# Kernel tuning notes

Measured on AMD Instinct MI355X. Metric: run time of the kernel, lower is better.

Reference implementation:

```python
import jax, jax.numpy as jnp
import numpy as np

MAP_X = 72; MAP_Y = 72      # global map grid
R = 300                      # number of rooms
MAXS = 8                     # rooms padded to 8x8 (zero-padded occupancy)
E = 32                       # room_embedding_width
N = 128                      # batch
CONV_CH = [64, 128, 256]; KS = [5, 3, 3]
FC = [512, 256]; OUT_W = 512


def setup_inputs() -> dict:
    key = jax.random.key(0)
    ks = jax.random.split(key, 20)
    rng = np.random.default_rng(0)
    widths = rng.integers(1, MAXS + 1, R)
    heights = rng.integers(1, MAXS + 1, R)
    # room_maps[i] is room.map transposed -> [width, height], zero-padded to [MAXS, MAXS]
    rm = np.zeros((R, MAXS, MAXS), np.int32)
    for i in range(R):
        rm[i, :widths[i], :heights[i]] = rng.integers(0, 2, (int(widths[i]), int(heights[i])))
    inp = {}
    # room top-left positions; rooms fit since max size is MAXS
    inp["X"] = jax.random.randint(ks[0], (N, R, 2), 0, MAP_X - MAXS + 1, dtype=jnp.int32)
    inp["room_maps"] = jnp.asarray(rm)
    inp["room_emb"] = jax.random.normal(ks[1], (R, E), jnp.float32)
    cin = [1 + E] + CONV_CH
    for i in range(3):
        k = KS[i]; fan = cin[i] * k * k
        inp[f"conv_w{i}"] = jax.random.normal(ks[2 + 2 * i], (cin[i + 1], cin[i], k, k), jnp.float32) / np.sqrt(fan).astype(np.float32)
        inp[f"conv_b{i}"] = jnp.zeros((cin[i + 1],), jnp.float32)
    fcd = [CONV_CH[-1]] + FC + [OUT_W]
    for i in range(3):
        inp[f"fc_w{i}"] = jax.random.normal(ks[10 + 2 * i], (fcd[i + 1], fcd[i]), jnp.float32) / np.sqrt(fcd[i]).astype(np.float32)
        inp[f"fc_b{i}"] = jnp.zeros((fcd[i + 1],), jnp.float32)
    return inp


def _encode_map(X, room_maps, room_emb):
    # Fused scatter: occupancy channel + embedding channels scattered in one pass.
    rm = room_maps.astype(room_emb.dtype)                    # [R, W, H]
    vals = jnp.concatenate(
        [rm[..., None], rm[..., None] * room_emb[:, None, None, :]], axis=-1
    )                                                        # [R, W, H, 1+E]
    ax = jnp.arange(MAXS)

    def one(pos):  # pos: [R, 2] positions for one batch element
        ix = jnp.broadcast_to(pos[:, 0, None, None] + ax[None, :, None], (R, MAXS, MAXS))
        iy = jnp.broadcast_to(pos[:, 1, None, None] + ax[None, None, :], (R, MAXS, MAXS))
        grid = jnp.zeros((MAP_X, MAP_Y, 1 + E), vals.dtype)
        # padded cells are zero so dropped/duplicate adds are exact
        return grid.at[ix, iy].add(vals, mode="drop")

    out = jax.vmap(one)(X)                                   # [N, MAP_X, MAP_Y, 1+E]
    # torch: transpose(1,3) -> [N, 1+E, MAP_Y, MAP_X]
    return jnp.transpose(out, (0, 3, 2, 1))


def _conv_relu(x, w, b, k):
    p = k // 2
    y = jax.lax.conv_general_dilated(
        x, w, (1, 1), [(p, p), (p, p)], dimension_numbers=("NCHW", "OIHW", "NCHW"))
    return jax.nn.relu(y + b[None, :, None, None])


def _maxpool3s2(x):
    return jax.lax.reduce_window(x, -jnp.inf, jax.lax.max, (1, 1, 3, 3), (1, 1, 2, 2), "VALID")


def reference(X, room_maps, room_emb, conv_w0, conv_b0, conv_w1, conv_b1, conv_w2, conv_b2, fc_w0, fc_b0, fc_w1, fc_b1, fc_w2, fc_b2):
    x = _encode_map(X, room_maps, room_emb)
    for w, b, k in ((conv_w0, conv_b0, KS[0]), (conv_w1, conv_b1, KS[1]), (conv_w2, conv_b2, KS[2])):
        x = _maxpool3s2(_conv_relu(x, w, b, k))
    x = jnp.mean(x, axis=(2, 3))                             # GlobalAvgPool2d
    x = jax.nn.relu(x @ fc_w0.T + fc_b0)
    x = jax.nn.relu(x @ fc_w1.T + fc_b1)
    return x @ fc_w2.T + fc_b2
```

## Files before the change

kernel.cpp:

```cpp
#include <hip/hip_runtime.h>
#include <hip/hip_bf16.h>
#include <cstdint>
#include <cstddef>

#define NB      128
#define RR      300
#define EMB     32

typedef __bf16 bf16x8 __attribute__((ext_vector_type(8)));
typedef float  f32x4  __attribute__((ext_vector_type(4)));
typedef unsigned short ushort8 __attribute__((ext_vector_type(8)));

__device__ __forceinline__ unsigned short f2bf(float f) {
    union { __hip_bfloat16 h; unsigned short u; } c;
    c.h = __float2bfloat16(f);
    return c.u;
}
__device__ __forceinline__ float bf2f(unsigned short u) {
    union { __hip_bfloat16 h; unsigned short u; } c;
    c.u = u;
    return __bfloat162float(c.h);
}

__device__ __forceinline__ void wpack_body(
    const float* __restrict__ w, unsigned short* __restrict__ wPT,
    int COUT, int CIN, int KK, int gpc, int idx, int total)
{
    if (idx >= total) return;
    int kk = idx & 31;
    int t  = idx >> 5;
    int oc = t % COUT;
    int kb = t / COUT;
    int g  = kb * 4 + (kk >> 3);
    int j  = kk & 7;
    int shift = g / gpc;
    int ci    = (g % gpc) * 8 + j;
    float v = (shift < KK && ci < CIN)
        ? w[(size_t)oc * CIN * KK + (size_t)ci * KK + shift] : 0.0f;
    wPT[idx] = f2bf(v);
}

__device__ __forceinline__ void fcT_body(
    const float* __restrict__ w, float* __restrict__ wT, int O, int I, int idx)
{
    if (idx >= O * I) return;
    int i = idx % I, o = idx / I;
    wT[(size_t)i * O + o] = w[idx];
}

__global__ __launch_bounds__(256) void prep_k(
    const int* __restrict__ rm, unsigned long long* __restrict__ masks,
    const float* __restrict__ cw0, unsigned short* __restrict__ WP0,
    const float* __restrict__ cw1, unsigned short* __restrict__ WP1,
    const float* __restrict__ cw2, unsigned short* __restrict__ WP2,
    int* __restrict__ kt0, int* __restrict__ kt1, int* __restrict__ kt2,
    const float* __restrict__ fw0, float* __restrict__ W0T,
    const float* __restrict__ fw1, float* __restrict__ W1T,
    const float* __restrict__ fw2, float* __restrict__ W2T)
{
    const int b = blockIdx.x;
    const int t = threadIdx.x;
    if (b < 2) {
        int r = b * 256 + t;
        if (r < RR) {
            unsigned long long m = 0ull;
            #pragma unroll
            for (int k = 0; k < 64; ++k)
                if (rm[r * 64 + k]) m |= (1ull << k);
            masks[r] = m;
        }
    } else if (b < 258) {
        wpack_body(cw0, WP0, 64, 33, 25, 5, (b - 2) * 256 + t, 32 * 64 * 32);
    } else if (b < 546) {
        wpack_body(cw1, WP1, 128, 64, 9, 8, (b - 258) * 256 + t, 18 * 128 * 32);
    } else if (b < 1698) {
        wpack_body(cw2, WP2, 256, 128, 9, 16, (b - 546) * 256 + t, 36 * 256 * 32);
    } else if (b < 1699) {
        #pragma unroll
        for (int which = 0; which < 3; ++which) {
            int ngr, gpc, K, Wp, CL;
            int* dst;
            if (which == 0)      { ngr = 128; gpc = 5;  K = 5; Wp = 20; CL = 40;  dst = kt0; }
            else if (which == 1) { ngr = 72;  gpc = 8;  K = 3; Wp = 37; CL = 72;  dst = kt1; }
            else                 { ngr = 144; gpc = 16; K = 3; Wp = 19; CL = 136; dst = kt2; }
            if (t < ngr) {
                int shift = t / gpc;
                int off = 0;
                if (shift < K * K) {
                    int ky = shift / K, kx = shift % K;
                    off = (ky * Wp + kx) * CL + (t % gpc) * 8;
                }
                dst[t] = off;
            }
        }
    } else if (b < 2211) {
        fcT_body(fw0, W0T, 512, 256, (b - 1699) * 256 + t);
    } else if (b < 2723) {
        fcT_body(fw1, W1T, 256, 512, (b - 2211) * 256 + t);
    } else {
        fcT_body(fw2, W2T, 512, 256, (b - 2723) * 256 + t);
    }
}

__device__ __forceinline__ void border_body(
    unsigned short* __restrict__ base, int Hp, int Wp, int CPG, int pad,
    int sampleStride, int nborder, int idx, int total)
{
    if (idx >= total) return;
    int c8 = idx % CPG;
    int t  = idx / CPG;
    int bi = t % nborder;
    int nl = t / nborder;

    int topN = pad * Wp;
    int y, x;
    if (bi < topN) {
        y = bi / Wp; x = bi - y * Wp;
    } else if (bi < 2 * topN) {
        int b2 = bi - topN;
        y = Hp - pad + b2 / Wp; x = b2 % Wp;
    } else {
        int mid = bi - 2 * topN;
        int rowlen = 2 * pad;
        y = pad + mid / rowlen;
        int r = mid % rowlen;
        x = r < pad ? r : Wp - pad + (r - pad);
    }
    uint4 z = make_uint4(0, 0, 0, 0);
    *reinterpret_cast<uint4*>(
        &base[((size_t)nl * sampleStride) +
              ((size_t)y * Wp + x) * (CPG * 8) + c8 * 8]) = z;
}

__global__ __launch_bounds__(512) void encode_k(
    const int* __restrict__ X, const unsigned long long* __restrict__ masks,
    const float* __restrict__ emb, unsigned short* __restrict__ G,
    int n0, int sampleStride)
{
    __shared__ float tile[4][72][33];
    __shared__ unsigned s_pos[RR];
    __shared__ unsigned long long s_mask[RR];
    __shared__ unsigned short s_list[320];
    __shared__ float s_emb[64 * 33];
    __shared__ int s_woff[8];
    __shared__ int s_cnt;

    const int nl = blockIdx.x, band = blockIdx.y;
    const int by = band * 4;
    const int n  = n0 + nl;
    const int tid = threadIdx.x;

    float* tf = &tile[0][0][0];
    for (int i = tid; i < 4 * 72 * 33; i += 512) tf[i] = 0.0f;

    const int2* Xp = reinterpret_cast<const int2*>(X);
    bool hot = false;
    if (tid < RR) {
        int2 pos = Xp[n * RR + tid];
        s_pos[tid]  = (unsigned)pos.x | ((unsigned)pos.y << 16);
        s_mask[tid] = masks[tid];
        hot = (pos.y <= by + 3) && (pos.y + 7 >= by);
    }
    unsigned long long bal = __ballot(hot);
    if ((tid & 63) == 0) s_woff[tid >> 6] = (int)__popcll(bal);
    __syncthreads();
    if (tid == 0) {
        int acc = 0;
        #pragma unroll
        for (int w = 0; w < 8; ++w) { int c = s_woff[w]; s_woff[w] = acc; acc += c; }
        s_cnt = acc;
    }
    __syncthreads();
    if (hot) {
        int w = tid >> 6, b = tid & 63;
        unsigned long long before = (b == 0) ? 0ull : (bal & ((1ull << b) - 1ull));
        s_list[s_woff[w] + (int)__popcll(before)] = (unsigned short)tid;
    }
    __syncthreads();

    const int lane = tid & 63;
    const int wvi  = tid >> 6;
    const int dx   = lane >> 3;
    const int c0   = (lane & 7) * 5;
    const int cnt  = s_cnt;

    for (int base = 0; base < cnt; base += 64) {
        int cn = cnt - base; if (cn > 64) cn = 64;
        for (int i = tid; i < cn * 33; i += 512) {
            int hi = i / 33, cc = i - hi * 33;
            int r = s_list[base + hi];
            s_emb[i] = (cc == 0) ? 1.0f : emb[r * EMB + cc - 1];
        }
        __syncthreads();

        int j = wvi;
        for (; j + 8 < cn; j += 16) {
            int rA = s_list[base + j];
            int rB = s_list[base + j + 8];
            unsigned pA = s_pos[rA], pB = s_pos[rB];
            unsigned long long mA = s_mask[rA] >> (dx * 8);
            unsigned long long mB = s_mask[rB] >> (dx * 8);
            int xA = (pA & 0xffff) + dx, yA = pA >> 16;
            int xB = (pB & 0xffff) + dx, yB = pB >> 16;
            float eA[5], eB[5];
            #pragma unroll
            for (int q = 0; q < 5; ++q) {
                eA[q] = (c0 + q < 33) ? s_emb[j * 33 + c0 + q] : 0.0f;
                eB[q] = (c0 + q < 33) ? s_emb[(j + 8) * 33 + c0 + q] : 0.0f;
            }
            #pragma unroll
            for (int dyb = 0; dyb < 4; ++dyb) {
                int dA = by + dyb - yA;
                if ((unsigned)dA < 8u && ((mA >> dA) & 1ull)) {
                    #pragma unroll
                    for (int q = 0; q < 5; ++q)
                        if (c0 + q < 33)
                            atomicAdd(&tile[dyb][xA][c0 + q], eA[q]);
                }
                int dB = by + dyb - yB;
                if ((unsigned)dB < 8u && ((mB >> dB) & 1ull)) {
                    #pragma unroll
                    for (int q = 0; q < 5; ++q)
                        if (c0 + q < 33)
                            atomicAdd(&tile[dyb][xB][c0 + q], eB[q]);
                }
            }
        }
        for (; j < cn; j += 8) {
            int r = s_list[base + j];
            unsigned pxy = s_pos[r];
            int px = pxy & 0xffff, py = pxy >> 16;
            unsigned long long mm = s_mask[r] >> (dx * 8);
            int x = px + dx;
            float ev[5];
            #pragma unroll
            for (int q = 0; q < 5; ++q)
                ev[q] = (c0 + q < 33) ? s_emb[j * 33 + c0 + q] : 0.0f;
            #pragma unroll
            for (int dyb = 0; dyb < 4; ++dyb) {
                int dyr = by + dyb - py;
                if ((unsigned)dyr < 8u && ((mm >> dyr) & 1ull)) {
                    #pragma unroll
                    for (int q = 0; q < 5; ++q)
                        if (c0 + q < 33)
                            atomicAdd(&tile[dyb][x][c0 + q], ev[q]);
                }
            }
        }
        __syncthreads();
    }
    __syncthreads();

    unsigned short* Gn = G + (size_t)nl * sampleStride;
    for (int i = tid; i < 4 * 72 * 10; i += 512) {
        int cc = i % 10;
        int t  = i / 10;
        int x  = t % 72;
        int dyb = t / 72;
        int c0w = cc * 4;
        unsigned short r[4];
        #pragma unroll
        for (int j = 0; j < 4; ++j)
            r[j] = (c0w + j < 33) ? f2bf(tile[dyb][x][c0w + j]) : 0;
        uint2 pk;
        pk.x = (unsigned)r[0] | ((unsigned)r[1] << 16);
        pk.y = (unsigned)r[2] | ((unsigned)r[3] << 16);
        *reinterpret_cast<uint2*>(
            &Gn[((size_t)(by + dyb + 2) * 76 + (x + 2)) * 40 + c0w]) = pk;
    }

    uint2 zz; zz.x = 0; zz.y = 0;
    for (int i = tid; i < 160; i += 512) {
        int cc = i % 10;
        int t  = i / 10;
        int ci = t & 3;
        int dyb = t >> 2;
        int x = ci < 2 ? ci : 72 + ci;
        *reinterpret_cast<uint2*>(
            &Gn[((size_t)(by + dyb + 2) * 76 + x) * 40 + cc * 4]) = zz;
    }
    if (band == 0 || band == 17) {
        int rbase = band == 0 ? 0 : 74;
        for (int i = tid; i < 2 * 76 * 10; i += 512) {
            int cc = i % 10;
            int t  = i / 10;
            int x  = t % 76;
            int r  = t / 76;
            *reinterpret_cast<uint2*>(
                &Gn[((size_t)(rbase + r) * 76 + x) * 40 + cc * 4]) = zz;
        }
    }
}

template<int KSTEPS>
__global__ __launch_bounds__(256, 3) void conv0_tile_k(
    const unsigned short* __restrict__ inP,
    const unsigned short* __restrict__ wPT,
    const int* __restrict__ ktab,
    const float* __restrict__ bias,
    unsigned short* __restrict__ out,
    int inSS, int outSS)
{
    constexpr int CL = 40;
    constexpr int LP = 72;
    __shared__ __align__(16) unsigned short slab[28 * 20 * CL];
    __shared__ __align__(16) unsigned short wbuf[2][2048];
    __shared__ int s_kt[KSTEPS * 4];
    unsigned short* s_c = slab;

    const int tid = threadIdx.x;
    const int tl  = blockIdx.x;
    const int nl  = blockIdx.y;
    const int tyi = tl / 5, txi = tl % 5;
    const int y0 = tyi * 24;
    const int x0 = txi < 4 ? txi * 16 : 56;

    const int lane = tid & 63, wv = tid >> 6, frow = lane & 15, fq = lane >> 4;

    if (tid < KSTEPS * 4) s_kt[tid] = ktab[tid];

    {
        const unsigned short* src = wPT + wv * 512 + lane * 8;
        __builtin_amdgcn_global_load_lds(
            (const __attribute__((address_space(1))) void*)src,
            (__attribute__((address_space(3))) void*)&wbuf[0][wv * 512],
            16, 0, 0);
    }

    const unsigned short* in_n = inP + (size_t)nl * inSS;
    {
        const uint4* src = reinterpret_cast<const uint4*>(in_n);
        uint4* dst = reinterpret_cast<uint4*>(slab);
        #pragma unroll
        for (int it = 0; it < 11; ++it) {
            int q = tid + it * 256;
            if (q < 2800) {
                int r = q / 100, c = q - r * 100;
                dst[q] = src[((y0 + r) * 76 + x0) * 5 + c];
            }
        }
    }

    int ldsb[6];
    #pragma unroll
    for (int mf = 0; mf < 6; ++mf)
        ldsb[mf] = ((mf * 4 + wv) * 20 + frow) * CL;

    f32x4 acc[6][4];
    #pragma unroll
    for (int a = 0; a < 6; ++a)
        #pragma unroll
        for (int b = 0; b < 4; ++b) acc[a][b] = (f32x4){0.f, 0.f, 0.f, 0.f};

    __syncthreads();

    #pragma unroll 2
    for (int kb = 0; kb < KSTEPS; ++kb) {
        const int cur = kb & 1;
        if (kb + 1 < KSTEPS) {
            const unsigned short* src =
                wPT + (size_t)(kb + 1) * 2048 + wv * 512 + lane * 8;
            __builtin_amdgcn_global_load_lds(
                (const __attribute__((address_space(1))) void*)src,
                (__attribute__((address_space(3))) void*)&wbuf[cur ^ 1][wv * 512],
                16, 0, 0);
        }
        int go = s_kt[kb * 4 + fq];
        bf16x8 af[6];
        #pragma unroll
        for (int mf = 0; mf < 6; ++mf)
            af[mf] = *reinterpret_cast<const bf16x8*>(&slab[ldsb[mf] + go]);
        const unsigned short* wl = &wbuf[cur][frow * 32 + fq * 8];
        #pragma unroll
        for (int ng = 0; ng < 4; ++ng) {
            bf16x8 bf = *reinterpret_cast<const bf16x8*>(&wl[ng * 512]);
            #pragma unroll
            for (int mf = 0; mf < 6; ++mf)
                acc[mf][ng] = __builtin_amdgcn_mfma_f32_16x16x32_bf16(
                    af[mf], bf, acc[mf][ng], 0, 0, 0);
        }
        __syncthreads();
    }

    unsigned short* out_n = out + (size_t)nl * outSS;
    const int erow = tid >> 2, eseg = tid & 3;
    #pragma unroll
    for (int mf = 0; mf < 6; ++mf) {
        __syncthreads();
        #pragma unroll
        for (int ng = 0; ng < 4; ++ng) {
            float bv = bias[ng * 16 + frow];
            #pragma unroll
            for (int j = 0; j < 4; ++j)
                s_c[(wv * 16 + fq * 4 + j) * LP + ng * 16 + frow] =
                    f2bf(fmaxf(acc[mf][ng][j] + bv, 0.0f));
        }
        __syncthreads();
        {
            int ty = mf * 4 + (erow >> 4);
            int tx = erow & 15;
            int pos = (y0 + ty) * 72 + (x0 + tx);
            ushort8 v0 = *reinterpret_cast<const ushort8*>(
                &s_c[erow * LP + eseg * 16]);
            ushort8 v1 = *reinterpret_cast<const ushort8*>(
                &s_c[erow * LP + eseg * 16 + 8]);
            unsigned short* op = out_n + (size_t)pos * 64 + eseg * 16;
            *reinterpret_cast<ushort8*>(op) = v0;
            *reinterpret_cast<ushort8*>(op + 8) = v1;
        }
    }
}

template<int MFRAG, int NG, int KH, int CPG, int CL, int SLAB, int KSTEPS>
__global__ __launch_bounds__(256, 2) void conv_mfma_k(
    const unsigned short* __restrict__ inP,
    const unsigned short* __restrict__ wPT,
    const int* __restrict__ ktab,
    const float* __restrict__ bias,
    unsigned short* __restrict__ out,
    int W, int Wp, int Mtot, int inSS, int outSS, int COUT)
{
    constexpr int Mblk = MFRAG * 64;
    constexpr int NOC  = NG * 16;
    constexpr int SEGS = NOC / 16;
    constexpr int LP   = NOC + 8;
    constexpr int CP   = CPG * 8;
    constexpr int CSZ  = Mblk * LP * 2;
    constexpr int SMEM = (SLAB * 2 > CSZ) ? SLAB * 2 : CSZ;
    __shared__ __align__(16) char smem[SMEM];
    __shared__ int s_kt[KSTEPS * 4];
    unsigned short* slab = reinterpret_cast<unsigned short*>(smem);
    unsigned short* s_c  = reinterpret_cast<unsigned short*>(smem);

    const int tid  = threadIdx.x;
    const int mb   = blockIdx.x;
    const int ocb  = blockIdx.y;
    const int nl   = blockIdx.z;
    const int lane = tid & 63;
    const int wv   = tid >> 6;
    const int frow = lane & 15;
    const int fq   = lane >> 4;

    if (tid < KSTEPS * 4) s_kt[tid] = ktab[tid];

    const int p0    = mb * Mblk;
    const int y0    = p0 / W;
    const int plast = (p0 + Mblk < Mtot ? p0 + Mblk : Mtot) - 1;
    const int rows  = plast / W - y0 + KH;

    const unsigned short* in_n =
        inP + (size_t)nl * inSS + (size_t)y0 * Wp * CP;
    const int nchunks = rows * Wp * CPG;
    for (int q = tid; q < nchunks; q += 256) {
        int pix = q / CPG, c8 = q - pix * CPG;
        uint4 v = reinterpret_cast<const uint4*>(in_n)[q];
        *reinterpret_cast<uint4*>(&slab[pix * CL + c8 * 8]) = v;
    }

    int ldsb[MFRAG];
    #pragma unroll
    for (int mf = 0; mf < MFRAG; ++mf) {
        int p  = p0 + mf * 64 + wv * 16 + frow;
        int pc = p < Mtot ? p : (Mtot - 1);
        int y  = pc / W;
        int x  = pc - y * W;
        ldsb[mf] = ((y - y0) * Wp + x) * CL;
    }
    const unsigned short* wbase =
        wPT + ((size_t)(ocb * NOC + frow)) * 32 + fq * 8;

    f32x4 acc[MFRAG][NG];
    #pragma unroll
    for (int mf = 0; mf < MFRAG; ++mf)
        #pragma unroll
        for (int ng = 0; ng < NG; ++ng)
            acc[mf][ng] = (f32x4){0.f, 0.f, 0.f, 0.f};

    __syncthreads();

    for (int kb = 0; kb < KSTEPS; ++kb) {
        int go = s_kt[kb * 4 + fq];
        bf16x8 af[MFRAG];
        #pragma unroll
        for (int mf = 0; mf < MFRAG; ++mf)
            af[mf] = *reinterpret_cast<const bf16x8*>(&slab[ldsb[mf] + go]);
        const unsigned short* wk = wbase + (size_t)kb * COUT * 32;
        #pragma unroll
        for (int ng = 0; ng < NG; ++ng) {
            bf16x8 bf = *reinterpret_cast<const bf16x8*>(wk + ng * 16 * 32);
            #pragma unroll
            for (int mf = 0; mf < MFRAG; ++mf)
                acc[mf][ng] = __builtin_amdgcn_mfma_f32_16x16x32_bf16(
                    af[mf], bf, acc[mf][ng], 0, 0, 0);
        }
    }

    __syncthreads();
    #pragma unroll
    for (int mf = 0; mf < MFRAG; ++mf) {
        #pragma unroll
        for (int ng = 0; ng < NG; ++ng) {
            float bv = bias[ocb * NOC + ng * 16 + frow];
            #pragma unroll
            for (int j = 0; j < 4; ++j)
                s_c[(mf * 64 + wv * 16 + fq * 4 + j) * LP + ng * 16 + frow] =
                    f2bf(fmaxf(acc[mf][ng][j] + bv, 0.0f));
        }
    }
    __syncthreads();
    unsigned short* out_n = out + (size_t)nl * outSS;
    for (int t = tid; t < Mblk * SEGS; t += 256) {
        int row = t / SEGS, seg = t - row * SEGS;
        int p = p0 + row;
        if (p < Mtot) {
            ushort8 v0 = *reinterpret_cast<const ushort8*>(
                &s_c[row * LP + seg * 16]);
            ushort8 v1 = *reinterpret_cast<const ushort8*>(
                &s_c[row * LP + seg * 16 + 8]);
            unsigned short* op =
                out_n + (size_t)p * COUT + ocb * NOC + seg * 16;
            *reinterpret_cast<ushort8*>(op) = v0;
            *reinterpret_cast<ushort8*>(op + 8) = v1;
        }
    }
}

__global__ __launch_bounds__(256) void pool_border_k(
    const unsigned short* __restrict__ in, unsigned short* __restrict__ out,
    int CG, int C, int W, int inSS,
    int HO, int WO, int Wpo, int outSS, int total,
    int npool, int bHp, int bWp, int bCPG, int bpad, int bnborder, int btotal)
{
    const int b = blockIdx.x;
    const int tidx = threadIdx.x;
    if (b >= npool) {
        border_body(out, bHp, bWp, bCPG, bpad, outSS, bnborder,
                    (b - npool) * 256 + tidx, btotal);
        return;
    }
    int idx = b * 256 + tidx;
    if (idx >= total) return;
    int cg = idx % CG;
    int t  = idx / CG;
    int x  = t % WO;
    t /= WO;
    int y  = t % HO;
    int nl = t / HO;

    const unsigned short* pin = in + (size_t)nl * inSS + cg * 8;
    ushort8 mx = {0,0,0,0,0,0,0,0};
    #pragma unroll
    for (int dy = 0; dy < 3; ++dy)
        #pragma unroll
        for (int dx = 0; dx < 3; ++dx) {
            ushort8 v = *reinterpret_cast<const ushort8*>(
                pin + ((size_t)(2 * y + dy) * W + (2 * x + dx)) * C);
            #pragma unroll
            for (int j = 0; j < 8; ++j) mx[j] = v[j] > mx[j] ? v[j] : mx[j];
        }
    *reinterpret_cast<ushort8*>(
        out + (size_t)nl * outSS +
        ((size_t)(y + 1) * Wpo + (x + 1)) * C + cg * 8) = mx;
}

__global__ __launch_bounds__(256) void pool2gap_k(
    const unsigned short* __restrict__ in, float* __restrict__ out,
    int inSS, int n0)
{
    __shared__ float red[4][4][8];
    const int nl = blockIdx.x;
    const int cg = blockIdx.y;
    const int tid = threadIdx.x;
    const int w  = tid >> 2;
    const int cq = tid & 3;
    const int y = w >> 3, x = w & 7;

    const unsigned short* p = in + (size_t)nl * inSS + cg * 32 + cq * 8;
    ushort8 mx = {0,0,0,0,0,0,0,0};
    #pragma unroll
    for (int dy = 0; dy < 3; ++dy)
        #pragma unroll
        for (int dx = 0; dx < 3; ++dx) {
            ushort8 v = *reinterpret_cast<const ushort8*>(
                p + ((size_t)(2 * y + dy) * 17 + (2 * x + dx)) * 256);
            #pragma unroll
            for (int j = 0; j < 8; ++j) mx[j] = v[j] > mx[j] ? v[j] : mx[j];
        }
    float s[8];
    #pragma unroll
    for (int j = 0; j < 8; ++j) s[j] = bf2f(mx[j]);
    #pragma unroll
    for (int m = 4; m < 64; m <<= 1)
        #pragma unroll
        for (int j = 0; j < 8; ++j)
            s[j] += __shfl_xor(s[j], m);
    if ((tid & 63) < 4) {
        #pragma unroll
        for (int j = 0; j < 8; ++j) red[tid >> 6][tid & 3][j] = s[j];
    }
    __syncthreads();
    if (tid < 32) {
        int cq2 = tid >> 3, j = tid & 7;
        float t = red[0][cq2][j] + red[1][cq2][j] + red[2][cq2][j] + red[3][cq2][j];
        out[(size_t)(n0 + nl) * 256 + cg * 32 + cq2 * 8 + j] = t * (1.0f / 64.0f);
    }
}

__global__ __launch_bounds__(256) void fc_fused_k(
    const float* __restrict__ in,
    const float* __restrict__ w0T, const float* __restrict__ b0,
    const float* __restrict__ w1T, const float* __restrict__ b1,
    const float* __restrict__ w2T, const float* __restrict__ b2,
    float* __restrict__ out)
{
    __shared__ float s_in[256], s_h0[512], s_h1[256];
    const int n = blockIdx.x, t = threadIdx.x;
    s_in[t] = in[(size_t)n * 256 + t];
    __syncthreads();
    float a0 = 0.f, a1 = 0.f;
    for (int i = 0; i < 256; ++i) {
        float v = s_in[i];
        a0 += v * w0T[i * 512 + t];
        a1 += v * w0T[i * 512 + t + 256];
    }
    s_h0[t]       = fmaxf(a0 + b0[t], 0.0f);
    s_h0[t + 256] = fmaxf(a1 + b0[t + 256], 0.0f);
    __syncthreads();
    float h = 0.f;
    for (int i = 0; i < 512; ++i) h += s_h0[i] * w1T[i * 256 + t];
    s_h1[t] = fmaxf(h + b1[t], 0.0f);
    __syncthreads();
    a0 = 0.f; a1 = 0.f;
    for (int i = 0; i < 256; ++i) {
        float v = s_h1[i];
        a0 += v * w2T[i * 512 + t];
        a1 += v * w2T[i * 512 + t + 256];
    }
    out[(size_t)n * 512 + t]       = a0 + b2[t];
    out[(size_t)n * 512 + t + 256] = a1 + b2[t + 256];
}

extern "C" void kernel_launch(void* const* d_in, const int* in_sizes, int n_in,
                              void* d_out, int out_size, void* d_ws, size_t ws_size,
                              hipStream_t stream)
{
    const int*   X   = (const int*)d_in[0];
    const int*   rm  = (const int*)d_in[1];
    const float* emb = (const float*)d_in[2];
    const float* cw0 = (const float*)d_in[3];
    const float* cb0 = (const float*)d_in[4];
    const float* cw1 = (const float*)d_in[5];
    const float* cb1 = (const float*)d_in[6];
    const float* cw2 = (const float*)d_in[7];
    const float* cb2 = (const float*)d_in[8];
    const float* fw0 = (const float*)d_in[9];
    const float* fb0 = (const float*)d_in[10];
    const float* fw1 = (const float*)d_in[11];
    const float* fb1 = (const float*)d_in[12];
    const float* fw2 = (const float*)d_in[13];
    const float* fb2 = (const float*)d_in[14];
    float* out = (float*)d_out;

    char* p = (char*)d_ws;
    auto alloc = [&](size_t bytes) -> char* {
        char* r = p; p += (bytes + 255) & ~(size_t)255; return r;
    };
    unsigned short* WP0 = (unsigned short*)alloc((size_t)32 * 64 * 32 * 2);
    unsigned short* WP1 = (unsigned short*)alloc((size_t)18 * 128 * 32 * 2);
    unsigned short* WP2 = (unsigned short*)alloc((size_t)36 * 256 * 32 * 2);
    int* KT0 = (int*)alloc(128 * 4);
    int* KT1 = (int*)alloc(72 * 4);
    int* KT2 = (int*)alloc(144 * 4);
    unsigned long long* MASKS = (unsigned long long*)alloc(RR * 8);
    float* W0T  = (float*)alloc((size_t)256 * 512 * 4);
    float* W1T  = (float*)alloc((size_t)512 * 256 * 4);
    float* W2T  = (float*)alloc((size_t)256 * 512 * 4);
    float* GAPB = (float*)alloc((size_t)NB * 256 * 4);
    size_t fixed_bytes = (size_t)(p - (char*)d_ws);

    const size_t A_FL = 231040, B_FL = 331776, C_FL = 133824;
    const size_t per_sample = (A_FL + B_FL + C_FL) * 2 + 768;
    int Bc = 128;
    while (Bc > 1 && fixed_bytes + (size_t)Bc * per_sample > ws_size) Bc >>= 1;

    unsigned short* bufA = (unsigned short*)alloc((size_t)Bc * A_FL * 2);
    unsigned short* bufC = (unsigned short*)alloc((size_t)Bc * C_FL * 2);
    unsigned short* bufB = (unsigned short*)alloc((size_t)Bc * B_FL * 2);

    prep_k<<<3235, 256, 0, stream>>>(
        rm, MASKS, cw0, WP0, cw1, WP1, cw2, WP2,
        KT0, KT1, KT2, fw0, W0T, fw1, W1T, fw2, W2T);

    for (int n0 = 0; n0 < NB; n0 += Bc) {
        encode_k<<<dim3(Bc, 18), 512, 0, stream>>>(X, MASKS, emb, bufA, n0, (int)A_FL);

        conv0_tile_k<32><<<dim3(15, Bc), 256, 0, stream>>>(
            bufA, WP0, KT0, cb0, bufB, (int)A_FL, (int)B_FL);

        {
            int total = Bc * 35 * 35 * 8;
            int npool = (total + 255) / 256;
            int btotal = Bc * 144 * 8;
            int nbord = (btotal + 255) / 256;
            pool_border_k<<<npool + nbord, 256, 0, stream>>>(
                bufB, bufC, 8, 64, 72, (int)B_FL,
                35, 35, 37, (int)C_FL, total,
                npool, 37, 37, 8, 1, 144, btotal);
        }

        conv_mfma_k<4, 8, 3, 8, 72, 29304, 18><<<dim3(5, 1, Bc), 256, 0, stream>>>(
            bufC, WP1, KT1, cb1, bufA, 35, 37,
            1225, (int)C_FL, (int)A_FL, 128);

        {
            int total = Bc * 17 * 17 * 16;
            int npool = (total + 255) / 256;
            int btotal = Bc * 72 * 16;
            int nbord = (btotal + 255) / 256;
            pool_border_k<<<npool + nbord, 256, 0, stream>>>(
                bufA, bufC + 87616, 16, 128, 35, (int)A_FL,
                17, 17, 19, (int)C_FL, total,
                npool, 19, 19, 16, 1, 72, btotal);
        }

        conv_mfma_k<5, 8, 3, 16, 136, 49096, 36><<<dim3(1, 2, Bc), 256, 0, stream>>>(
            bufC + 87616, WP2, KT2, cb2, bufB, 17, 19,
            289, (int)C_FL, (int)B_FL, 256);

        pool2gap_k<<<dim3(Bc, 8), 256, 0, stream>>>(bufB, GAPB, (int)B_FL, n0);
    }

    fc_fused_k<<<NB, 256, 0, stream>>>(GAPB, W0T, fb0, W1T, fb1, W2T, fb2, out);
}
```

Before: 458.0 us.

## Replace atomic scatter in map encoder with per-pixel gather over candidate rooms

The encode kernel now assigns one thread per output pixel in an 8-row band and loops over the rooms overlapping that band, accumulating the 33-channel embedding in registers instead of atomically adding into a shared tile. Embeddings for all rooms are staged once in shared memory padded to 36 floats for vector loads, and outputs are written as 16-byte stores. This removes shared-memory atomic contention and the tile zeroing and readback, but every thread scans every candidate room in its band, and the grid shrinks to half as many larger blocks.

Measured after the change: 420.1 us. 8.3% less time.

```diff
diff --git a/kernel.cpp b/kernel.cpp
--- a/kernel.cpp
+++ b/kernel.cpp
@@ -132,26 +132,30 @@
               ((size_t)y * Wp + x) * (CPG * 8) + c8 * 8]) = z;
 }
 
-__global__ __launch_bounds__(512) void encode_k(
+__global__ __launch_bounds__(576) void encode_k(
     const int* __restrict__ X, const unsigned long long* __restrict__ masks,
     const float* __restrict__ emb, unsigned short* __restrict__ G,
     int n0, int sampleStride)
 {
-    __shared__ float tile[4][72][33];
+    __shared__ float s_emb[RR * 36];
     __shared__ unsigned s_pos[RR];
     __shared__ unsigned long long s_mask[RR];
     __shared__ unsigned short s_list[320];
-    __shared__ float s_emb[64 * 33];
-    __shared__ int s_woff[8];
+    __shared__ int s_woff[9];
     __shared__ int s_cnt;
 
     const int nl = blockIdx.x, band = blockIdx.y;
-    const int by = band * 4;
+    const int by = band * 8;
     const int n  = n0 + nl;
     const int tid = threadIdx.x;
 
-    float* tf = &tile[0][0][0];
-    for (int i = tid; i < 4 * 72 * 33; i += 512) tf[i] = 0.0f;
+    for (int i = tid; i < RR * 36; i += 576) {
+        int r = i / 36, c = i - r * 36;
+        float v = 0.0f;
+        if (c == 0) v = 1.0f;
+        else if (c < 33) v = emb[r * EMB + c - 1];
+        s_emb[i] = v;
+    }
 
     const int2* Xp = reinterpret_cast<const int2*>(X);
     bool hot = false;
@@ -159,7 +163,7 @@
         int2 pos = Xp[n * RR + tid];
         s_pos[tid]  = (unsigned)pos.x | ((unsigned)pos.y << 16);
         s_mask[tid] = masks[tid];
-        hot = (pos.y <= by + 3) && (pos.y + 7 >= by);
+        hot = (pos.y <= by + 7) && (pos.y + 7 >= by);
     }
     unsigned long long bal = __ballot(hot);
     if ((tid & 63) == 0) s_woff[tid >> 6] = (int)__popcll(bal);
@@ -167,7 +171,7 @@
     if (tid == 0) {
         int acc = 0;
         #pragma unroll
-        for (int w = 0; w < 8; ++w) { int c = s_woff[w]; s_woff[w] = acc; acc += c; }
+        for (int w = 0; w < 9; ++w) { int c = s_woff[w]; s_woff[w] = acc; acc += c; }
         s_cnt = acc;
     }
     __syncthreads();
@@ -178,116 +182,61 @@
     }
     __syncthreads();
 
-    const int lane = tid & 63;
-    const int wvi  = tid >> 6;
-    const int dx   = lane >> 3;
-    const int c0   = (lane & 7) * 5;
-    const int cnt  = s_cnt;
-
-    for (int base = 0; base < cnt; base += 64) {
-        int cn = cnt - base; if (cn > 64) cn = 64;
-        for (int i = tid; i < cn * 33; i += 512) {
-            int hi = i / 33, cc = i - hi * 33;
-            int r = s_list[base + hi];
-            s_emb[i] = (cc == 0) ? 1.0f : emb[r * EMB + cc - 1];
-        }
-        __syncthreads();
-
-        int j = wvi;
-        for (; j + 8 < cn; j += 16) {
-            int rA = s_list[base + j];
-            int rB = s_list[base + j + 8];
-            unsigned pA = s_pos[rA], pB = s_pos[rB];
-            unsigned long long mA = s_mask[rA] >> (dx * 8);
-            unsigned long long mB = s_mask[rB] >> (dx * 8);
-            int xA = (pA & 0xffff) + dx, yA = pA >> 16;
-            int xB = (pB & 0xffff) + dx, yB = pB >> 16;
-            float eA[5], eB[5];
-            #pragma unroll
-            for (int q = 0; q < 5; ++q) {
-                eA[q] = (c0 + q < 33) ? s_emb[j * 33 + c0 + q] : 0.0f;
-                eB[q] = (c0 + q < 33) ? s_emb[(j + 8) * 33 + c0 + q] : 0.0f;
-            }
-            #pragma unroll
-            for (int dyb = 0; dyb < 4; ++dyb) {
-                int dA = by + dyb - yA;
-                if ((unsigned)dA < 8u && ((mA >> dA) & 1ull)) {
-                    #pragma unroll
-                    for (int q = 0; q < 5; ++q)
-                        if (c0 + q < 33)
-                            atomicAdd(&tile[dyb][xA][c0 + q], eA[q]);
-                }
-                int dB = by + dyb - yB;
-                if ((unsigned)dB < 8u && ((mB >> dB) & 1ull)) {
-                    #pragma unroll
-                    for (int q = 0; q < 5; ++q)
-                        if (c0 + q < 33)
-                            atomicAdd(&tile[dyb][xB][c0 + q], eB[q]);
-                }
-            }
-        }
-        for (; j < cn; j += 8) {
-            int r = s_list[base + j];
-            unsigned pxy = s_pos[r];
-            int px = pxy & 0xffff, py = pxy >> 16;
-            unsigned long long mm = s_mask[r] >> (dx * 8);
-            int x = px + dx;
-            float ev[5];
-            #pragma unroll
-            for (int q = 0; q < 5; ++q)
-                ev[q] = (c0 + q < 33) ? s_emb[j * 33 + c0 + q] : 0.0f;
-            #pragma unroll
-            for (int dyb = 0; dyb < 4; ++dyb) {
-                int dyr = by + dyb - py;
-                if ((unsigned)dyr < 8u && ((mm >> dyr) & 1ull)) {
-                    #pragma unroll
-                    for (int q = 0; q < 5; ++q)
-                        if (c0 + q < 33)
-                            atomicAdd(&tile[dyb][x][c0 + q], ev[q]);
-                }
-            }
-        }
-        __syncthreads();
-    }
-    __syncthreads();
+    const int x  = tid % 72;
+    const int Y  = by + tid / 72;
+
+    f32x4 acc[9];
+    #pragma unroll
+    for (int k = 0; k < 9; ++k) acc[k] = (f32x4){0.f, 0.f, 0.f, 0.f};
+
+    const int cnt = s_cnt;
+    for (int idx = 0; idx < cnt; ++idx) {
+        int r = s_list[idx];
+        unsigned pxy = s_pos[r];
+        int dxr = x - (int)(pxy & 0xffffu);
+        int dyr = Y - (int)(pxy >> 16);
+        if (((unsigned)dxr < 8u) && ((unsigned)dyr < 8u) &&
+            ((s_mask[r] >> (dxr * 8 + dyr)) & 1ull)) {
+            const f32x4* er = reinterpret_cast<const f32x4*>(&s_emb[r * 36]);
+            #pragma unroll
+            for (int k = 0; k < 9; ++k) acc[k] += er[k];
+        }
+    }
 
     unsigned short* Gn = G + (size_t)nl * sampleStride;
-    for (int i = tid; i < 4 * 72 * 10; i += 512) {
-        int cc = i % 10;
-        int t  = i / 10;
-        int x  = t % 72;
-        int dyb = t / 72;
-        int c0w = cc * 4;
-        unsigned short r[4];
-        #pragma unroll
-        for (int j = 0; j < 4; ++j)
-            r[j] = (c0w + j < 33) ? f2bf(tile[dyb][x][c0w + j]) : 0;
-        uint2 pk;
-        pk.x = (unsigned)r[0] | ((unsigned)r[1] << 16);
-        pk.y = (unsigned)r[2] | ((unsigned)r[3] << 16);
-        *reinterpret_cast<uint2*>(
-            &Gn[((size_t)(by + dyb + 2) * 76 + (x + 2)) * 40 + c0w]) = pk;
-    }
-
-    uint2 zz; zz.x = 0; zz.y = 0;
-    for (int i = tid; i < 160; i += 512) {
-        int cc = i % 10;
-        int t  = i / 10;
-        int ci = t & 3;
-        int dyb = t >> 2;
-        int x = ci < 2 ? ci : 72 + ci;
-        *reinterpret_cast<uint2*>(
-            &Gn[((size_t)(by + dyb + 2) * 76 + x) * 40 + cc * 4]) = zz;
-    }
-    if (band == 0 || band == 17) {
+    {
+        unsigned short o[40];
+        #pragma unroll
+        for (int k = 0; k < 9; ++k)
+            #pragma unroll
+            for (int j = 0; j < 4; ++j)
+                o[k * 4 + j] = f2bf(acc[k][j]);
+        #pragma unroll
+        for (int c = 36; c < 40; ++c) o[c] = 0;
+        uint4* dst = reinterpret_cast<uint4*>(
+            &Gn[((size_t)(Y + 2) * 76 + (x + 2)) * 40]);
+        const uint4* src = reinterpret_cast<const uint4*>(o);
+        #pragma unroll
+        for (int q = 0; q < 5; ++q) dst[q] = src[q];
+    }
+
+    uint4 zz4; zz4.x = zz4.y = zz4.z = zz4.w = 0;
+    if (tid < 160) {
+        int q = tid % 5, cell = tid / 5;
+        int ci = cell & 3, rr = cell >> 2;
+        int xx = ci < 2 ? ci : 72 + ci;
+        uint4* dst = reinterpret_cast<uint4*>(
+            &Gn[((size_t)(by + rr + 2) * 76 + xx) * 40]);
+        dst[q] = zz4;
+    }
+    if (band == 0 || band == 8) {
         int rbase = band == 0 ? 0 : 74;
-        for (int i = tid; i < 2 * 76 * 10; i += 512) {
-            int cc = i % 10;
-            int t  = i / 10;
-            int x  = t % 76;
-            int r  = t / 76;
-            *reinterpret_cast<uint2*>(
-                &Gn[((size_t)(rbase + r) * 76 + x) * 40 + cc * 4]) = zz;
+        for (int i = tid; i < 2 * 76 * 5; i += 576) {
+            int q = i % 5, cell = i / 5;
+            int xx = cell % 76, rr = cell / 76;
+            uint4* dst = reinterpret_cast<uint4*>(
+                &Gn[((size_t)(rbase + rr) * 76 + xx) * 40]);
+            dst[q] = zz4;
         }
     }
 }
@@ -692,7 +641,7 @@
         KT0, KT1, KT2, fw0, W0T, fw1, W1T, fw2, W2T);
 
     for (int n0 = 0; n0 < NB; n0 += Bc) {
-        encode_k<<<dim3(Bc, 18), 512, 0, stream>>>(X, MASKS, emb, bufA, n0, (int)A_FL);
+        encode_k<<<dim3(Bc, 9), 576, 0, stream>>>(X, MASKS, emb, bufA, n0, (int)A_FL);
 
         conv0_tile_k<32><<<dim3(15, Bc), 256, 0, stream>>>(
             bufA, WP0, KT0, cb0, bufB, (int)A_FL, (int)B_FL);
```
